# Kernel tuning notes

Measured on AMD Instinct MI355X. Metric: run time of the kernel, lower is better.

Reference implementation:

```python
import jax, jax.numpy as jnp
import numpy as np

B, E, C = 1024, 512, 16384
MRG, ALPHA, V, K, LAM, TAU = 0.1, 32.0, 100.0, 1.0, 0.1, 1.5


def _l2norm(x):
    # matches torch l2_norm: divide by sqrt(sum(x^2) + 1e-12) row-wise
    n = jnp.sqrt(jnp.sum(x * x, axis=1) + 1e-12)
    return x / n[:, None]


def setup_inputs() -> dict:
    key = jax.random.key(0)
    k1, k2, k3, k4, k5 = jax.random.split(key, 5)
    inputsBatch = _l2norm(jax.random.normal(k1, (B, E), dtype=jnp.float32))
    targetsBatch = jax.random.randint(k2, (B,), 0, C, dtype=jnp.int32)
    # kaiming_normal fan_out on (C, E): std = sqrt(2 / E)
    proxies = jax.random.normal(k3, (C, E), dtype=jnp.float32) * np.sqrt(2.0 / E).astype(np.float32)
    effectiveNum = jax.random.uniform(k4, (C,), dtype=jnp.float32) * 100.0
    learnedSim = jax.random.uniform(k5, (C,), dtype=jnp.float32)
    return {"inputsBatch": inputsBatch, "targetsBatch": targetsBatch,
            "proxies": proxies, "effectiveNum": effectiveNum, "learnedSim": learnedSim}


def reference(inputsBatch, targetsBatch, proxies, effectiveNum, learnedSim):
    nb_classes = proxies.shape[0]
    P = jax.nn.one_hot(targetsBatch, nb_classes, dtype=inputsBatch.dtype)  # [B, C]
    N = 1.0 - P
    proxy_l2 = _l2norm(proxies)
    cos = inputsBatch @ proxy_l2.T  # [B, C]

    classCnt = P.sum(axis=0)                      # [C]
    present = (classCnt > 0).astype(cos.dtype)

    w_base = 1.0 / (1.0 + jnp.log1p(effectiveNum))
    eta = (1.0 + K * (1.0 - learnedSim)) * w_base + LAM
    outlierSim = learnedSim - eta                 # [C]

    # enableFilter=False: mask at positive positions stays 1, so each present
    # class contributes mean(ones)=1 to pos_weight_sum
    pos_weight_sum = jnp.sum(present)

    # negative-position adaptive reweighting (vectorized over the class loop)
    neg_vals = jnp.where(cos < outlierSim[None, :],
                         (1.0 / jnp.maximum(1.0, effectiveNum))[None, :],
                         1.0)                      # [B, C]
    Ncnt = N.sum(axis=0)
    neg_mean = jnp.sum(N * neg_vals, axis=0) / jnp.maximum(Ncnt, 1.0)
    neg_weight_sum = jnp.sum(jnp.where(Ncnt > 0, neg_mean, 0.0))

    mask = jnp.where(N > 0, neg_vals, 1.0)        # 1 at positive entries

    pos_term = jnp.sum(jnp.log1p(jnp.sum(P * jnp.exp(ALPHA * (MRG - cos) * mask), axis=0)))
    neg_term = jnp.sum(jnp.log1p(jnp.sum(N * jnp.exp(ALPHA * (cos + MRG) * mask), axis=0)))

    return pos_term / pos_weight_sum + neg_term / neg_weight_sum
```

## Files before the change

### kernel.cpp

```cpp
#include <hip/hip_runtime.h>
#include <math.h>

#define B_SZ 1024
#define E_SZ 512
#define C_SZ 16384
#define MRG 0.1f
#define ALPHA 32.0f
#define A2LOG2E 46.16624090918536f
#define K_HY 1.0f
#define LAM 0.1f

#define BM 256
#define BN 256
#define BK 64

typedef __bf16 bf16;
typedef bf16 bf16x8 __attribute__((ext_vector_type(8)));
typedef float f32x4 __attribute__((ext_vector_type(4)));

__device__ __forceinline__ void async16(const void* g, void* l) {
    __builtin_amdgcn_global_load_lds(
        (const __attribute__((address_space(1))) void*)g,
        (__attribute__((address_space(3))) void*)l,
        16, 0, 0);
}

__global__ __launch_bounds__(256) void prep_fused(
    const float* __restrict__ proxies, bf16* __restrict__ Pbf,
    const float* __restrict__ inputs, bf16* __restrict__ Abf,
    const float* __restrict__ effNum, const float* __restrict__ lSim,
    float* __restrict__ oSim, float* __restrict__ iEff,
    float* __restrict__ zeroBase) {
    const int blk = blockIdx.x;
    const int tid = threadIdx.x;
    if (blk < 4096) {
        int row = blk * 4 + (tid >> 6);
        int lane = tid & 63;
        const float* pr = proxies + (size_t)row * E_SZ + lane * 8;
        float4 v0 = *(const float4*)pr;
        float4 v1 = *(const float4*)(pr + 4);
        float ss = v0.x * v0.x + v0.y * v0.y + v0.z * v0.z + v0.w * v0.w +
                   v1.x * v1.x + v1.y * v1.y + v1.z * v1.z + v1.w * v1.w;
#pragma unroll
        for (int m = 1; m < 64; m <<= 1) ss += __shfl_xor(ss, m);
        float inv = 1.0f / sqrtf(ss + 1e-12f);
        bf16x8 o;
        o[0] = (bf16)(v0.x * inv); o[1] = (bf16)(v0.y * inv);
        o[2] = (bf16)(v0.z * inv); o[3] = (bf16)(v0.w * inv);
        o[4] = (bf16)(v1.x * inv); o[5] = (bf16)(v1.y * inv);
        o[6] = (bf16)(v1.z * inv); o[7] = (bf16)(v1.w * inv);
        *(bf16x8*)(Pbf + (size_t)row * E_SZ + lane * 8) = o;
    } else if (blk < 4352) {
        int i = ((blk - 4096) * 256 + tid) * 8;
        float4 v0 = *(const float4*)(inputs + i);
        float4 v1 = *(const float4*)(inputs + i + 4);
        bf16x8 o;
        o[0] = (bf16)v0.x; o[1] = (bf16)v0.y; o[2] = (bf16)v0.z; o[3] = (bf16)v0.w;
        o[4] = (bf16)v1.x; o[5] = (bf16)v1.y; o[6] = (bf16)v1.z; o[7] = (bf16)v1.w;
        *(bf16x8*)(Abf + i) = o;
    } else if (blk < 4416) {
        int c = (blk - 4352) * 256 + tid;
        float en = effNum[c], ls = lSim[c];
        float wb = 1.0f / (1.0f + log1pf(en));
        float eta = (1.0f + K_HY * (1.0f - ls)) * wb + LAM;
        oSim[c] = ls - eta;
        iEff[c] = 1.0f / fmaxf(1.0f, en);
    } else {
        int i = (blk - 4416) * 256 + tid;
        if (i < 16386) {
            float4 z = {0.f, 0.f, 0.f, 0.f};
            *(float4*)(zeroBase + (size_t)i * 4) = z;
        }
    }
}

__global__ __launch_bounds__(512, 2) void gemm_epilogue(
    const bf16* __restrict__ Abf,
    const bf16* __restrict__ Pbf,
    const int* __restrict__ targets,
    const float* __restrict__ oSimA,
    const float* __restrict__ iEffA,
    float* __restrict__ posExp,
    float* __restrict__ negExp,
    float* __restrict__ negVals,
    int* __restrict__ cCnt) {
    __shared__ __align__(16) bf16 Alds[2][BM * BK];
    __shared__ __align__(16) bf16 Blds[2][BN * BK];
    __shared__ int tgtLds[BM];
    __shared__ float scratch[2 * BN];

    const int tid = threadIdx.x;
    const int wave = tid >> 6, lane = tid & 63;
    const int quad = lane >> 4, l16 = lane & 15;
    const int wm = wave >> 2, wn = wave & 3;
    const int bn0 = blockIdx.x * BN, bm0 = blockIdx.y * BM;

    if (tid < BM) tgtLds[tid] = targets[bm0 + tid];

    f32x4 zero = {0.f, 0.f, 0.f, 0.f};
    f32x4 acc[8][4];
#pragma unroll
    for (int i = 0; i < 8; ++i)
#pragma unroll
        for (int j = 0; j < 4; ++j) acc[i][j] = zero;

    const int sRow = tid >> 3;
    const int sSlot = (tid & 7) ^ (sRow & 7);
    const bf16* gA = Abf + (size_t)(bm0 + sRow) * E_SZ + sSlot * 8;
    const bf16* gB = Pbf + (size_t)(bn0 + sRow) * E_SZ + sSlot * 8;
    const int ldsChunk = wave * 512;

    int aOff[8], bOff[4], sl[2];
#pragma unroll
    for (int mi = 0; mi < 8; ++mi)
        aOff[mi] = (wm * 128 + mi * 16 + l16) * BK;
#pragma unroll
    for (int ni = 0; ni < 4; ++ni)
        bOff[ni] = (wn * 64 + ni * 16 + l16) * BK;
#pragma unroll
    for (int kh = 0; kh < 2; ++kh)
        sl[kh] = ((kh * 4 + quad) ^ (l16 & 7)) * 8;

    __syncthreads();

#pragma unroll
    for (int rnd = 0; rnd < 4; ++rnd)
        async16(gA + (size_t)rnd * 64 * E_SZ, &Alds[0][rnd * 4096 + ldsChunk]);
#pragma unroll
    for (int rnd = 0; rnd < 4; ++rnd)
        async16(gB + (size_t)rnd * 64 * E_SZ, &Blds[0][rnd * 4096 + ldsChunk]);

#pragma unroll
    for (int t = 0; t < 8; ++t) {
        const int cur = t & 1;
        __builtin_amdgcn_s_barrier();
        __builtin_amdgcn_sched_barrier(0);
        if (t < 7) {
            const int kOff = (t + 1) * BK;
#pragma unroll
            for (int rnd = 0; rnd < 4; ++rnd)
                async16(gA + (size_t)rnd * 64 * E_SZ + kOff,
                        &Alds[1 - cur][rnd * 4096 + ldsChunk]);
#pragma unroll
            for (int rnd = 0; rnd < 4; ++rnd)
                async16(gB + (size_t)rnd * 64 * E_SZ + kOff,
                        &Blds[1 - cur][rnd * 4096 + ldsChunk]);
            asm volatile("s_waitcnt vmcnt(8)" ::: "memory");
        } else {
            asm volatile("s_waitcnt vmcnt(0)" ::: "memory");
        }
        __builtin_amdgcn_s_barrier();
        __builtin_amdgcn_sched_barrier(0);

#pragma unroll
        for (int kh = 0; kh < 2; ++kh) {
            bf16x8 af[8], bf_[4];
#pragma unroll
            for (int mi = 0; mi < 8; ++mi)
                af[mi] = *(const bf16x8*)&Alds[cur][aOff[mi] + sl[kh]];
#pragma unroll
            for (int ni = 0; ni < 4; ++ni)
                bf_[ni] = *(const bf16x8*)&Blds[cur][bOff[ni] + sl[kh]];
#pragma unroll
            for (int mi = 0; mi < 8; ++mi)
#pragma unroll
                for (int ni = 0; ni < 4; ++ni)
                    acc[mi][ni] = __builtin_amdgcn_mfma_f32_16x16x32_bf16(
                        af[mi], bf_[ni], acc[mi][ni], 0, 0, 0);
        }
    }
    __builtin_amdgcn_sched_barrier(0);

    int colG[4];
    float oS[4], iE[4];
#pragma unroll
    for (int ni = 0; ni < 4; ++ni) {
        colG[ni] = bn0 + wn * 64 + ni * 16 + l16;
        oS[ni] = oSimA[colG[ni]];
        iE[ni] = iEffA[colG[ni]];
    }
    float negE[4] = {0.f, 0.f, 0.f, 0.f};
    float negV[4] = {0.f, 0.f, 0.f, 0.f};
#pragma unroll
    for (int mi = 0; mi < 8; ++mi) {
#pragma unroll
        for (int r = 0; r < 4; ++r) {
            int rowL = wm * 128 + mi * 16 + quad * 4 + r;
            int tgt = tgtLds[rowL];
#pragma unroll
            for (int ni = 0; ni < 4; ++ni) {
                float cosv = acc[mi][ni][r];
                if (tgt == colG[ni]) {
                    atomicAdd(&posExp[colG[ni]],
                              __builtin_amdgcn_exp2f(A2LOG2E * (MRG - cosv)));
                    atomicAdd(&cCnt[colG[ni]], 1);
                } else {
                    float nv = (cosv < oS[ni]) ? iE[ni] : 1.0f;
                    negE[ni] += __builtin_amdgcn_exp2f(A2LOG2E * (cosv + MRG) * nv);
                    negV[ni] += nv;
                }
            }
        }
    }
#pragma unroll
    for (int ni = 0; ni < 4; ++ni) {
        negE[ni] += __shfl_xor(negE[ni], 16); negE[ni] += __shfl_xor(negE[ni], 32);
        negV[ni] += __shfl_xor(negV[ni], 16); negV[ni] += __shfl_xor(negV[ni], 32);
    }
    float* nEsh = scratch;
    float* nVsh = scratch + BN;
    scratch[tid] = 0.0f;
    __syncthreads();
    if (quad == 0) {
#pragma unroll
        for (int ni = 0; ni < 4; ++ni) {
            int cl = wn * 64 + ni * 16 + l16;
            atomicAdd(&nEsh[cl], negE[ni]);
            atomicAdd(&nVsh[cl], negV[ni]);
        }
    }
    __syncthreads();
    if (tid < BN) {
        atomicAdd(&negExp[bn0 + tid], nEsh[tid]);
        atomicAdd(&negVals[bn0 + tid], nVsh[tid]);
    }
}

__global__ __launch_bounds__(256) void finalize(
    const float* __restrict__ posExp, const float* __restrict__ negExp,
    const float* __restrict__ negVals, const int* __restrict__ cCnt,
    float* __restrict__ acc4, int* __restrict__ counter,
    float* __restrict__ out) {
    const int tid = threadIdx.x;
    float pt = 0.f, nt = 0.f, pws = 0.f, nws = 0.f;
#pragma unroll
    for (int j = 0; j < 4; ++j) {
        int c = blockIdx.x * 1024 + j * 256 + tid;
        pt += log1pf(posExp[c]);
        nt += log1pf(negExp[c]);
        int cnt = cCnt[c];
        pws += (cnt > 0) ? 1.0f : 0.0f;
        int Nc = B_SZ - cnt;
        nws += (Nc > 0) ? negVals[c] / (float)Nc : 0.0f;
    }
#pragma unroll
    for (int m = 1; m < 64; m <<= 1) {
        pt += __shfl_xor(pt, m);
        nt += __shfl_xor(nt, m);
        pws += __shfl_xor(pws, m);
        nws += __shfl_xor(nws, m);
    }
    __shared__ float red[4][4];
    int wv = tid >> 6;
    if ((tid & 63) == 0) {
        red[wv][0] = pt; red[wv][1] = nt; red[wv][2] = pws; red[wv][3] = nws;
    }
    __syncthreads();
    if (tid < 4) {
        float s = red[0][tid] + red[1][tid] + red[2][tid] + red[3][tid];
        atomicAdd(&acc4[tid], s);
    }
    __syncthreads();
    __threadfence();
    if (tid == 0) {
        int ticket = atomicAdd(counter, 1);
        if (ticket == 15) {
            float a0 = atomicAdd(&acc4[0], 0.0f);
            float a1 = atomicAdd(&acc4[1], 0.0f);
            float a2 = atomicAdd(&acc4[2], 0.0f);
            float a3 = atomicAdd(&acc4[3], 0.0f);
            out[0] = a0 / a2 + a1 / a3;
        }
    }
}

extern "C" void kernel_launch(void* const* d_in, const int* in_sizes, int n_in,
                              void* d_out, int out_size, void* d_ws, size_t ws_size,
                              hipStream_t stream) {
    const float* inputs = (const float*)d_in[0];
    const int* targets = (const int*)d_in[1];
    const float* proxies = (const float*)d_in[2];
    const float* effNum = (const float*)d_in[3];
    const float* lSim = (const float*)d_in[4];
    float* out = (float*)d_out;

    bf16* Pbf = (bf16*)d_ws;
    bf16* Abf = Pbf + (size_t)C_SZ * E_SZ;
    float* oSim = (float*)(Abf + (size_t)B_SZ * E_SZ);
    float* iEff = oSim + C_SZ;
    float* posExp = iEff + C_SZ;
    float* negExp = posExp + C_SZ;
    float* negVals = negExp + C_SZ;
    int* cCnt = (int*)(negVals + C_SZ);
    float* acc4 = (float*)(cCnt + C_SZ);
    int* counter = (int*)(acc4 + 4);

    prep_fused<<<4481, 256, 0, stream>>>(proxies, Pbf, inputs, Abf,
                                         effNum, lSim, oSim, iEff, posExp);
    gemm_epilogue<<<dim3(C_SZ / BN, B_SZ / BM), 512, 0, stream>>>(
        Abf, Pbf, targets, oSim, iEff, posExp, negExp, negVals, cCnt);
    finalize<<<16, 256, 0, stream>>>(posExp, negExp, negVals, cCnt,
                                     acc4, counter, out);
}
```

Before: 116.9 us.

## Restructure GEMM main loop into half-K stages with ping-pong MFMA/LDS phases

Splits each 64-wide K tile into two 32-wide LDS halves and reorganizes the main loop into four barrier-separated phases. In each phase, LDS reads for one 128-row quarter are interleaved with async global loads for future half-tiles, and the MFMA groups run at raised wave priority (s_setprio). The goal is to overlap global loads, LDS reads and matrix math more finely across waves. In exchange it drops the XOR swizzle, which may cause LDS bank conflicts, and adds many barriers per iteration.

```diff
diff --git a/kernel.cpp b/kernel.cpp
--- a/kernel.cpp
+++ b/kernel.cpp
@@ -84,8 +84,8 @@
     float* __restrict__ negExp,
     float* __restrict__ negVals,
     int* __restrict__ cCnt) {
-    __shared__ __align__(16) bf16 Alds[2][BM * BK];
-    __shared__ __align__(16) bf16 Blds[2][BN * BK];
+    __shared__ __align__(16) bf16 Alds[2][2][256 * 32];
+    __shared__ __align__(16) bf16 Blds[2][2][256 * 32];
     __shared__ int tgtLds[BM];
     __shared__ float scratch[2 * BN];
 
@@ -104,70 +104,79 @@
 #pragma unroll
         for (int j = 0; j < 4; ++j) acc[i][j] = zero;
 
-    const int sRow = tid >> 3;
-    const int sSlot = (tid & 7) ^ (sRow & 7);
-    const bf16* gA = Abf + (size_t)(bm0 + sRow) * E_SZ + sSlot * 8;
-    const bf16* gB = Pbf + (size_t)(bn0 + sRow) * E_SZ + sSlot * 8;
-    const int ldsChunk = wave * 512;
-
-    int aOff[8], bOff[4], sl[2];
-#pragma unroll
-    for (int mi = 0; mi < 8; ++mi)
-        aOff[mi] = (wm * 128 + mi * 16 + l16) * BK;
-#pragma unroll
-    for (int ni = 0; ni < 4; ++ni)
-        bOff[ni] = (wn * 64 + ni * 16 + l16) * BK;
-#pragma unroll
-    for (int kh = 0; kh < 2; ++kh)
-        sl[kh] = ((kh * 4 + quad) ^ (l16 & 7)) * 8;
-
-    __syncthreads();
-
-#pragma unroll
-    for (int rnd = 0; rnd < 4; ++rnd)
-        async16(gA + (size_t)rnd * 64 * E_SZ, &Alds[0][rnd * 4096 + ldsChunk]);
-#pragma unroll
-    for (int rnd = 0; rnd < 4; ++rnd)
-        async16(gB + (size_t)rnd * 64 * E_SZ, &Blds[0][rnd * 4096 + ldsChunk]);
-
+    const bf16* gAs = Abf + (size_t)(bm0 + (tid >> 2)) * E_SZ + (tid & 3) * 8;
+    const bf16* gBs = Pbf + (size_t)(bn0 + (tid >> 2)) * E_SZ + (tid & 3) * 8;
+
+    const int aBase = (wm * 128 + l16) * 32 + quad * 8;
+    const int bBase = (wn * 64 + l16) * 32 + quad * 8;
+
+#define BARX() do { __builtin_amdgcn_s_barrier(); \
+                    __builtin_amdgcn_sched_barrier(0); } while (0)
+
+#define STAGE_AB(dst, kh, kt) do {                                          \
+    _Pragma("unroll")                                                       \
+    for (int rnd = 0; rnd < 2; ++rnd) {                                     \
+        async16(gAs + (size_t)rnd * 128 * E_SZ + (kt) * 64 + (kh) * 32,     \
+                &Alds[dst][kh][rnd * 4096 + wave * 512]);                   \
+        async16(gBs + (size_t)rnd * 128 * E_SZ + (kt) * 64 + (kh) * 32,     \
+                &Blds[dst][kh][rnd * 4096 + wave * 512]);                   \
+    }                                                                       \
+} while (0)
+
+#define DS_READ(cur, mh, kk) do {                                           \
+    const bf16* pA = &Alds[cur][kk][0];                                     \
+    const bf16* pB = &Blds[cur][kk][0];                                     \
+    _Pragma("unroll")                                                       \
+    for (int mi = 0; mi < 4; ++mi)                                          \
+        af[mi] = *(const bf16x8*)(pA + aBase + ((mh) * 4 + mi) * 512);      \
+    _Pragma("unroll")                                                       \
+    for (int ni = 0; ni < 4; ++ni)                                          \
+        bfr[ni] = *(const bf16x8*)(pB + bBase + ni * 512);                  \
+} while (0)
+
+#define MFMA_Q(mh) do {                                                     \
+    __builtin_amdgcn_s_setprio(1);                                          \
+    _Pragma("unroll")                                                       \
+    for (int mi = 0; mi < 4; ++mi)                                          \
+        _Pragma("unroll")                                                   \
+        for (int ni = 0; ni < 4; ++ni)                                      \
+            acc[(mh) * 4 + mi][ni] = __builtin_amdgcn_mfma_f32_16x16x32_bf16( \
+                af[mi], bfr[ni], acc[(mh) * 4 + mi][ni], 0, 0, 0);          \
+    __builtin_amdgcn_s_setprio(0);                                          \
+} while (0)
+
+    __syncthreads();
+
+    STAGE_AB(0, 0, 0);
+    STAGE_AB(0, 1, 0);
+    STAGE_AB(1, 0, 1);
+    asm volatile("s_waitcnt vmcnt(4)" ::: "memory");
+    BARX();
+
+    bf16x8 af[4], bfr[4];
 #pragma unroll
     for (int t = 0; t < 8; ++t) {
-        const int cur = t & 1;
-        __builtin_amdgcn_s_barrier();
-        __builtin_amdgcn_sched_barrier(0);
-        if (t < 7) {
-            const int kOff = (t + 1) * BK;
-#pragma unroll
-            for (int rnd = 0; rnd < 4; ++rnd)
-                async16(gA + (size_t)rnd * 64 * E_SZ + kOff,
-                        &Alds[1 - cur][rnd * 4096 + ldsChunk]);
-#pragma unroll
-            for (int rnd = 0; rnd < 4; ++rnd)
-                async16(gB + (size_t)rnd * 64 * E_SZ + kOff,
-                        &Blds[1 - cur][rnd * 4096 + ldsChunk]);
-            asm volatile("s_waitcnt vmcnt(8)" ::: "memory");
-        } else {
-            asm volatile("s_waitcnt vmcnt(0)" ::: "memory");
-        }
-        __builtin_amdgcn_s_barrier();
-        __builtin_amdgcn_sched_barrier(0);
-
-#pragma unroll
-        for (int kh = 0; kh < 2; ++kh) {
-            bf16x8 af[8], bf_[4];
-#pragma unroll
-            for (int mi = 0; mi < 8; ++mi)
-                af[mi] = *(const bf16x8*)&Alds[cur][aOff[mi] + sl[kh]];
-#pragma unroll
-            for (int ni = 0; ni < 4; ++ni)
-                bf_[ni] = *(const bf16x8*)&Blds[cur][bOff[ni] + sl[kh]];
-#pragma unroll
-            for (int mi = 0; mi < 8; ++mi)
-#pragma unroll
-                for (int ni = 0; ni < 4; ++ni)
-                    acc[mi][ni] = __builtin_amdgcn_mfma_f32_16x16x32_bf16(
-                        af[mi], bf_[ni], acc[mi][ni], 0, 0, 0);
-        }
+        const int cur = t & 1, nxt = cur ^ 1;
+        DS_READ(cur, 0, 0);
+        if (t + 1 < 8) STAGE_AB(nxt, 1, t + 1);
+        BARX();
+        MFMA_Q(0);
+        BARX();
+        DS_READ(cur, 1, 0);
+        BARX();
+        MFMA_Q(1);
+        BARX();
+        DS_READ(cur, 0, 1);
+        if (t + 2 < 8) STAGE_AB(cur, 0, t + 2);
+        BARX();
+        MFMA_Q(0);
+        BARX();
+        DS_READ(cur, 1, 1);
+        if (t < 6) asm volatile("s_waitcnt vmcnt(4)" ::: "memory");
+        else       asm volatile("s_waitcnt vmcnt(0)" ::: "memory");
+        BARX();
+        MFMA_Q(1);
+        BARX();
     }
     __builtin_amdgcn_sched_barrier(0);
 
@@ -224,6 +233,10 @@
         atomicAdd(&negExp[bn0 + tid], nEsh[tid]);
         atomicAdd(&negVals[bn0 + tid], nVsh[tid]);
     }
+#undef BARX
+#undef STAGE_AB
+#undef DS_READ
+#undef MFMA_Q
 }
 
 __global__ __launch_bounds__(256) void finalize(
```

Result: slower. 123.5 us (+5.6%).

## Shrink GEMM tile to 128x256x32 and raise occupancy to four blocks per CU

Applied to the files above, without the earlier changes.

Halves the M tile and the K step. Each wave now holds a 4x4 MFMA accumulator block instead of 8x4, so launch bounds can request four blocks per CU. The LDS loading drops the XOR swizzle and uses a simple row-major layout with three async loads per stage. The aim is more resident waves to hide latency and more blocks across the GPU, at the cost of more K iterations and barriers, lower per-wave reuse, possible LDS bank conflicts without the swizzle, and twice as many blocks issuing global atomics in the epilogue. The host launch grid must also change to match BM=128, which is not shown.

```diff
diff --git a/kernel.cpp b/kernel.cpp
--- a/kernel.cpp
+++ b/kernel.cpp
@@ -10,9 +10,10 @@
 #define K_HY 1.0f
 #define LAM 0.1f
 
-#define BM 256
+#define BM 128
 #define BN 256
-#define BK 64
+#define BK 32
+#define NT (E_SZ / BK)
 
 typedef __bf16 bf16;
 typedef bf16 bf16x8 __attribute__((ext_vector_type(8)));
@@ -74,7 +75,7 @@
     }
 }
 
-__global__ __launch_bounds__(512, 2) void gemm_epilogue(
+__global__ __launch_bounds__(512, 4) void gemm_epilogue(
     const bf16* __restrict__ Abf,
     const bf16* __restrict__ Pbf,
     const int* __restrict__ targets,
@@ -98,76 +99,54 @@
     if (tid < BM) tgtLds[tid] = targets[bm0 + tid];
 
     f32x4 zero = {0.f, 0.f, 0.f, 0.f};
-    f32x4 acc[8][4];
-#pragma unroll
-    for (int i = 0; i < 8; ++i)
+    f32x4 acc[4][4];
+#pragma unroll
+    for (int i = 0; i < 4; ++i)
 #pragma unroll
         for (int j = 0; j < 4; ++j) acc[i][j] = zero;
 
-    const int sRow = tid >> 3;
-    const int sSlot = (tid & 7) ^ (sRow & 7);
-    const bf16* gA = Abf + (size_t)(bm0 + sRow) * E_SZ + sSlot * 8;
-    const bf16* gB = Pbf + (size_t)(bn0 + sRow) * E_SZ + sSlot * 8;
-    const int ldsChunk = wave * 512;
-
-    int aOff[8], bOff[4], sl[2];
-#pragma unroll
-    for (int mi = 0; mi < 8; ++mi)
-        aOff[mi] = (wm * 128 + mi * 16 + l16) * BK;
-#pragma unroll
-    for (int ni = 0; ni < 4; ++ni)
-        bOff[ni] = (wn * 64 + ni * 16 + l16) * BK;
-#pragma unroll
-    for (int kh = 0; kh < 2; ++kh)
-        sl[kh] = ((kh * 4 + quad) ^ (l16 & 7)) * 8;
-
-    __syncthreads();
-
-#pragma unroll
-    for (int rnd = 0; rnd < 4; ++rnd)
-        async16(gA + (size_t)rnd * 64 * E_SZ, &Alds[0][rnd * 4096 + ldsChunk]);
-#pragma unroll
-    for (int rnd = 0; rnd < 4; ++rnd)
-        async16(gB + (size_t)rnd * 64 * E_SZ, &Blds[0][rnd * 4096 + ldsChunk]);
-
-#pragma unroll
-    for (int t = 0; t < 8; ++t) {
+    const bf16* gAs = Abf + (size_t)(bm0 + (tid >> 2)) * E_SZ + (tid & 3) * 8;
+    const bf16* gBs = Pbf + (size_t)(bn0 + (tid >> 2)) * E_SZ + (tid & 3) * 8;
+
+    const int aBase = (wm * 64 + l16) * BK + quad * 8;
+    const int bBase = (wn * 64 + l16) * BK + quad * 8;
+
+    __syncthreads();
+
+    async16(gAs, &Alds[0][tid * 8]);
+    async16(gBs, &Blds[0][tid * 8]);
+    async16(gBs + (size_t)128 * E_SZ, &Blds[0][4096 + tid * 8]);
+
+#pragma unroll
+    for (int t = 0; t < NT; ++t) {
         const int cur = t & 1;
         __builtin_amdgcn_s_barrier();
         __builtin_amdgcn_sched_barrier(0);
-        if (t < 7) {
+        if (t < NT - 1) {
             const int kOff = (t + 1) * BK;
-#pragma unroll
-            for (int rnd = 0; rnd < 4; ++rnd)
-                async16(gA + (size_t)rnd * 64 * E_SZ + kOff,
-                        &Alds[1 - cur][rnd * 4096 + ldsChunk]);
-#pragma unroll
-            for (int rnd = 0; rnd < 4; ++rnd)
-                async16(gB + (size_t)rnd * 64 * E_SZ + kOff,
-                        &Blds[1 - cur][rnd * 4096 + ldsChunk]);
-            asm volatile("s_waitcnt vmcnt(8)" ::: "memory");
+            async16(gAs + kOff, &Alds[1 - cur][tid * 8]);
+            async16(gBs + kOff, &Blds[1 - cur][tid * 8]);
+            async16(gBs + (size_t)128 * E_SZ + kOff, &Blds[1 - cur][4096 + tid * 8]);
+            asm volatile("s_waitcnt vmcnt(3)" ::: "memory");
         } else {
             asm volatile("s_waitcnt vmcnt(0)" ::: "memory");
         }
         __builtin_amdgcn_s_barrier();
         __builtin_amdgcn_sched_barrier(0);
 
-#pragma unroll
-        for (int kh = 0; kh < 2; ++kh) {
-            bf16x8 af[8], bf_[4];
-#pragma unroll
-            for (int mi = 0; mi < 8; ++mi)
-                af[mi] = *(const bf16x8*)&Alds[cur][aOff[mi] + sl[kh]];
+        bf16x8 af[4], bfr[4];
+#pragma unroll
+        for (int mi = 0; mi < 4; ++mi)
+            af[mi] = *(const bf16x8*)&Alds[cur][aBase + mi * 16 * BK];
+#pragma unroll
+        for (int ni = 0; ni < 4; ++ni)
+            bfr[ni] = *(const bf16x8*)&Blds[cur][bBase + ni * 16 * BK];
+#pragma unroll
+        for (int mi = 0; mi < 4; ++mi)
 #pragma unroll
             for (int ni = 0; ni < 4; ++ni)
-                bf_[ni] = *(const bf16x8*)&Blds[cur][bOff[ni] + sl[kh]];
-#pragma unroll
-            for (int mi = 0; mi < 8; ++mi)
-#pragma unroll
-                for (int ni = 0; ni < 4; ++ni)
-                    acc[mi][ni] = __builtin_amdgcn_mfma_f32_16x16x32_bf16(
-                        af[mi], bf_[ni], acc[mi][ni], 0, 0, 0);
-        }
+                acc[mi][ni] = __builtin_amdgcn_mfma_f32_16x16x32_bf16(
+                    af[mi], bfr[ni], acc[mi][ni], 0, 0, 0);
     }
     __builtin_amdgcn_sched_barrier(0);
 
@@ -182,10 +161,10 @@
     float negE[4] = {0.f, 0.f, 0.f, 0.f};
     float negV[4] = {0.f, 0.f, 0.f, 0.f};
 #pragma unroll
-    for (int mi = 0; mi < 8; ++mi) {
+    for (int mi = 0; mi < 4; ++mi) {
 #pragma unroll
         for (int r = 0; r < 4; ++r) {
-            int rowL = wm * 128 + mi * 16 + quad * 4 + r;
+            int rowL = wm * 64 + mi * 16 + quad * 4 + r;
             int tgt = tgtLds[rowL];
 #pragma unroll
             for (int ni = 0; ni < 4; ++ni) {
@@ -209,7 +188,7 @@
     }
     float* nEsh = scratch;
     float* nVsh = scratch + BN;
-    scratch[tid] = 0.0f;
+    scratch[tid & 511] = 0.0f;
     __syncthreads();
     if (quad == 0) {
 #pragma unroll
```

Result: no change. 117.1 us (median of 2 runs) (+0.2%).
